# Kernel optimization log

Hardware: AMD Instinct MI355X
Metric: run time of the kernel (lower is better)

Reference implementation:

```python
import jax, jax.numpy as jnp
import numpy as np

N_NODES = 100000
D = 256
N_EDGES = 3200000
NEG_SLOPE = 0.01  # torch F.leaky_relu default


def setup_inputs() -> dict:
    key = jax.random.key(0)
    ks = jax.random.split(key, 5)
    x = jax.random.normal(ks[0], (N_NODES, D), dtype=jnp.float32)
    edge_rows = jax.random.randint(ks[1], (N_EDGES,), 0, N_NODES, dtype=jnp.int32)
    edge_cols = jax.random.randint(ks[2], (N_EDGES,), 0, N_NODES, dtype=jnp.int32)
    edge_vals = jax.random.uniform(ks[3], (N_EDGES,), dtype=jnp.float32)
    # Linear(dim, dim) with xavier_normal_ weight, default bias init ~ U(-1/sqrt(d), 1/sqrt(d))
    std = float(np.sqrt(2.0 / (D + D)))
    W_w = jax.random.normal(ks[4], (D, D), dtype=jnp.float32) * std
    W_b = jnp.zeros((D,), dtype=jnp.float32)
    return {"x": x, "edge_rows": edge_rows, "edge_cols": edge_cols,
            "edge_vals": edge_vals, "W_w": W_w, "W_b": W_b}


def reference(x, edge_rows, edge_cols, edge_vals, W_w, W_b):
    # h = W(x)  (torch Linear: x @ W^T + b)
    h = jnp.einsum('nd,ed->ne', x, W_w) + W_b  # [n, d]
    # SpMM: out[r] = sum_e A[r, c_e] * h[c_e]  via gather + segment_sum
    msgs = edge_vals[:, None] * h[edge_cols]  # [n_edges, d]
    agg = jax.ops.segment_sum(msgs, edge_rows, num_segments=x.shape[0])  # [n, d]
    return jnp.where(agg >= 0, agg, NEG_SLOPE * agg)
```

## Files before the change

### kernel.cpp

```cpp
#include <hip/hip_runtime.h>
#include <stdint.h>

#define DIM 256
#define NEG_SLOPE 0.01f

#define NBLK 512
#define MAXK 400
#define ROWS_PER_BUCKET 256

typedef float    vfloat4 __attribute__((ext_vector_type(4)));
typedef _Float16 vhalf4  __attribute__((ext_vector_type(4)));
typedef _Float16 half8   __attribute__((ext_vector_type(8)));
typedef float    floatx4 __attribute__((ext_vector_type(4)));
typedef unsigned int vuint2 __attribute__((ext_vector_type(2)));


#define MBM 128
#define MBN 64
#define MBK 32
#define MLDP 40

__global__ __launch_bounds__(256) void gemm_xwT_kernel(
        const float* __restrict__ x, const float* __restrict__ W,
        const float* __restrict__ bias, _Float16* __restrict__ h, int M) {
    __shared__ _Float16 Ax[MBM][MLDP];
    __shared__ _Float16 Bw[MBN][MLDP];

    const int tid  = (int)threadIdx.x;
    const int row0 = blockIdx.y * MBM;
    const int col0 = blockIdx.x * MBN;
    const int wid  = tid >> 6;
    const int lane = tid & 63;
    const int wr = wid >> 1;
    const int wc = wid & 1;
    const int fr = lane & 15;
    const int fk = (lane >> 4) * 8;

    const int arow = tid >> 1;
    const int ak   = (tid & 1) * 16;
    const int wrow = tid >> 2;
    const int wk   = (tid & 3) * 8;

    floatx4 acc[4][2];
#pragma unroll
    for (int m = 0; m < 4; ++m)
#pragma unroll
        for (int n = 0; n < 2; ++n) acc[m][n] = (floatx4){0.f, 0.f, 0.f, 0.f};

    for (int kk = 0; kk < DIM; kk += MBK) {
        {
            int grow = row0 + arow;
            const float* src = &x[(size_t)grow * DIM + kk + ak];
            half8 h0, h1;
            if (grow < M) {
                vfloat4 f0 = *(const vfloat4*)(src + 0);
                vfloat4 f1 = *(const vfloat4*)(src + 4);
                vfloat4 f2 = *(const vfloat4*)(src + 8);
                vfloat4 f3 = *(const vfloat4*)(src + 12);
                h0 = (half8){(_Float16)f0.x, (_Float16)f0.y, (_Float16)f0.z, (_Float16)f0.w,
                             (_Float16)f1.x, (_Float16)f1.y, (_Float16)f1.z, (_Float16)f1.w};
                h1 = (half8){(_Float16)f2.x, (_Float16)f2.y, (_Float16)f2.z, (_Float16)f2.w,
                             (_Float16)f3.x, (_Float16)f3.y, (_Float16)f3.z, (_Float16)f3.w};
            } else {
                h0 = (half8)(_Float16)0; h1 = (half8)(_Float16)0;
            }
            *(half8*)&Ax[arow][ak]     = h0;
            *(half8*)&Ax[arow][ak + 8] = h1;
        }
        {
            const float* src = &W[(size_t)(col0 + wrow) * DIM + kk + wk];
            vfloat4 f0 = *(const vfloat4*)(src + 0);
            vfloat4 f1 = *(const vfloat4*)(src + 4);
            half8 hb = (half8){(_Float16)f0.x, (_Float16)f0.y, (_Float16)f0.z, (_Float16)f0.w,
                               (_Float16)f1.x, (_Float16)f1.y, (_Float16)f1.z, (_Float16)f1.w};
            *(half8*)&Bw[wrow][wk] = hb;
        }
        __syncthreads();

        half8 a[4], b[2];
#pragma unroll
        for (int m = 0; m < 4; ++m)
            a[m] = *(const half8*)&Ax[wr * 64 + m * 16 + fr][fk];
#pragma unroll
        for (int n = 0; n < 2; ++n)
            b[n] = *(const half8*)&Bw[wc * 32 + n * 16 + fr][fk];
#pragma unroll
        for (int m = 0; m < 4; ++m)
#pragma unroll
            for (int n = 0; n < 2; ++n)
                acc[m][n] = __builtin_amdgcn_mfma_f32_16x16x32_f16(a[m], b[n], acc[m][n], 0, 0, 0);
        __syncthreads();
    }

#pragma unroll
    for (int m = 0; m < 4; ++m) {
#pragma unroll
        for (int n = 0; n < 2; ++n) {
            int col = col0 + wc * 32 + n * 16 + fr;
            float bv = bias[col];
#pragma unroll
            for (int j = 0; j < 4; ++j) {
                int row = row0 + wr * 64 + m * 16 + (lane >> 4) * 4 + j;
                if (row < M)
                    h[(size_t)row * DIM + col] = (_Float16)(acc[m][n][j] + bv);
            }
        }
    }
}


__device__ inline int wave_incl_scan(int v) {
    const int lane = threadIdx.x & 63;
#pragma unroll
    for (int off = 1; off < 64; off <<= 1) {
        int t = __shfl_up(v, off, 64);
        if (lane >= off) v += t;
    }
    return v;
}


__global__ __launch_bounds__(256) void hist2_kernel(const int* __restrict__ rows,
        int* __restrict__ hist2, int E, int K, int chunk) {
    __shared__ int lh[MAXK];
    const int tid = (int)threadIdx.x;
    const int b = (int)blockIdx.x;
    for (int i = tid; i < K; i += 256) lh[i] = 0;
    __syncthreads();
    const int beg = b * chunk;
    const int end = min(beg + chunk, E);
    for (int i = beg + tid; i < end; i += 256)
        atomicAdd(&lh[__builtin_nontemporal_load(&rows[i]) >> 8], 1);
    __syncthreads();
    for (int i = tid; i < K; i += 256) hist2[i * NBLK + b] = lh[i];
}

__global__ __launch_bounds__(256) void scanA_kernel(int* __restrict__ hist2,
        int* __restrict__ total, int K) {
    __shared__ int wtot[4];
    const int tid = (int)threadIdx.x;
    const int lane = tid & 63, wid = tid >> 6;
    const int k = (int)blockIdx.x;
    int* row = &hist2[k * NBLK];
    int v0 = row[tid * 2], v1 = row[tid * 2 + 1];
    int s = v0 + v1;
    int incl = wave_incl_scan(s);
    if (lane == 63) wtot[wid] = incl;
    __syncthreads();
    int woff = 0;
    for (int ww = 0; ww < wid; ++ww) woff += wtot[ww];
    int excl = woff + incl - s;
    row[tid * 2] = excl;
    row[tid * 2 + 1] = excl + v0;
    if (tid == 255) total[k] = woff + incl;
}

__global__ __launch_bounds__(64) void scanB_kernel(const int* __restrict__ total,
        int* __restrict__ bbase, int K) {
    const int lane = (int)threadIdx.x;
    int run = 0;
    for (int b = 0; b < K; b += 64) {
        int i = b + lane;
        int v = (i < K) ? total[i] : 0;
        int incl = wave_incl_scan(v);
        if (i < K) bbase[i] = run + incl - v;
        run += __shfl(incl, 63, 64);
    }
}

__global__ __launch_bounds__(256) void coarse_scatter_kernel(
        const int* __restrict__ rows, const int* __restrict__ cols,
        const float* __restrict__ vals, const int* __restrict__ hist2,
        const int* __restrict__ bbase, vuint2* __restrict__ coarse,
        int E, int K, int chunk) {
    __shared__ int cur[MAXK];
    const int tid = (int)threadIdx.x;
    const int b = (int)blockIdx.x;
    for (int i = tid; i < K; i += 256) cur[i] = bbase[i] + hist2[i * NBLK + b];
    __syncthreads();
    const int beg = b * chunk;
    const int end = min(beg + chunk, E);
    for (int i = beg + tid; i < end; i += 256) {
        int r = __builtin_nontemporal_load(&rows[i]);
        int c = __builtin_nontemporal_load(&cols[i]);
        float v = __builtin_nontemporal_load(&vals[i]);
        int pos = atomicAdd(&cur[r >> 8], 1);
        vuint2 rec;
        rec.x = ((unsigned)(r & 255) << 18) | (unsigned)c;
        rec.y = __float_as_uint(v);
        coarse[pos] = rec;
    }
}

__global__ __launch_bounds__(256) void fine_sort_kernel(
        const vuint2* __restrict__ coarse, const int* __restrict__ bbase,
        vuint2* __restrict__ sorted, int* __restrict__ offs,
        int N, int E, int K) {
    __shared__ int lh[ROWS_PER_BUCKET];
    __shared__ int wtot[4];
    const int tid = (int)threadIdx.x;
    const int lane = tid & 63, wid = tid >> 6;
    const int k = (int)blockIdx.x;
    const int row0 = k * ROWS_PER_BUCKET;
    const int beg = bbase[k];
    const int end = (k + 1 < K) ? bbase[k + 1] : E;
    lh[tid] = 0;
    __syncthreads();
    for (int j = beg + tid; j < end; j += 256)
        atomicAdd(&lh[coarse[j].x >> 18], 1);
    __syncthreads();
    int v = lh[tid];
    int incl = wave_incl_scan(v);
    if (lane == 63) wtot[wid] = incl;
    __syncthreads();
    int woff = 0;
    for (int ww = 0; ww < wid; ++ww) woff += wtot[ww];
    int excl = woff + incl - v;
    lh[tid] = beg + excl;
    if (row0 + tid < N) offs[row0 + tid] = beg + excl;
    __syncthreads();
    for (int j = beg + tid; j < end; j += 256) {
        vuint2 rec = __builtin_nontemporal_load(&coarse[j]);
        int pos = atomicAdd(&lh[rec.x >> 18], 1);
        sorted[pos] = rec;
    }
}


__global__ __launch_bounds__(256) void agg_kernel(
        const _Float16* __restrict__ h, const vuint2* __restrict__ sorted,
        const int* __restrict__ offs, float* __restrict__ out, int N, int E) {
    const int node = blockIdx.x * 4 + ((int)threadIdx.x >> 6);
    if (node >= N) return;
    const int lane = (int)threadIdx.x & 63;
    const int beg = offs[node];
    const int end = (node + 1 < N) ? offs[node + 1] : E;

    float4 acc0 = make_float4(0.f, 0.f, 0.f, 0.f);
    float4 acc1 = make_float4(0.f, 0.f, 0.f, 0.f);

    int j = beg;
    for (; j + 7 < end; j += 8) {
        vuint2 cv[8];
        vhalf4 hv[8];
#pragma unroll
        for (int u = 0; u < 8; ++u) cv[u] = __builtin_nontemporal_load(&sorted[j + u]);
#pragma unroll
        for (int u = 0; u < 8; ++u)
            hv[u] = *(const vhalf4*)(&h[(size_t)(cv[u].x & 0x3FFFF) * DIM + lane * 4]);
#pragma unroll
        for (int u = 0; u < 8; ++u) {
            float v = __uint_as_float(cv[u].y);
            float4* a = (u & 1) ? &acc1 : &acc0;
            a->x += v * (float)hv[u].x;
            a->y += v * (float)hv[u].y;
            a->z += v * (float)hv[u].z;
            a->w += v * (float)hv[u].w;
        }
    }
    for (; j < end; ++j) {
        vuint2 cv = __builtin_nontemporal_load(&sorted[j]);
        float v = __uint_as_float(cv.y);
        vhalf4 hv = *(const vhalf4*)(&h[(size_t)(cv.x & 0x3FFFF) * DIM + lane * 4]);
        acc0.x += v * (float)hv.x; acc0.y += v * (float)hv.y;
        acc0.z += v * (float)hv.z; acc0.w += v * (float)hv.w;
    }
    vfloat4 a;
    a.x = acc0.x + acc1.x;
    a.y = acc0.y + acc1.y;
    a.z = acc0.z + acc1.z;
    a.w = acc0.w + acc1.w;
    a.x = (a.x >= 0.f) ? a.x : NEG_SLOPE * a.x;
    a.y = (a.y >= 0.f) ? a.y : NEG_SLOPE * a.y;
    a.z = (a.z >= 0.f) ? a.z : NEG_SLOPE * a.z;
    a.w = (a.w >= 0.f) ? a.w : NEG_SLOPE * a.w;
    __builtin_nontemporal_store(a, (vfloat4*)(&out[(size_t)node * DIM + lane * 4]));
}


__global__ __launch_bounds__(256) void zero_f32_kernel(float* __restrict__ p, long long n) {
    long long i = (long long)blockIdx.x * blockDim.x + threadIdx.x;
    long long stride = (long long)gridDim.x * blockDim.x;
    for (; i < n; i += stride) p[i] = 0.0f;
}

__global__ __launch_bounds__(64) void edge_atomic_kernel(
        const int* __restrict__ rows, const int* __restrict__ cols,
        const float* __restrict__ vals, const _Float16* __restrict__ h,
        float* __restrict__ out, int E) {
    const int e = blockIdx.x;
    if (e >= E) return;
    const int lane = threadIdx.x;
    const int r = rows[e];
    const int c = cols[e];
    const float v = vals[e];
    vhalf4 hv = *(const vhalf4*)(&h[(size_t)c * DIM + lane * 4]);
    float* dst = &out[(size_t)r * DIM + lane * 4];
    atomicAdd(dst + 0, v * (float)hv.x);
    atomicAdd(dst + 1, v * (float)hv.y);
    atomicAdd(dst + 2, v * (float)hv.z);
    atomicAdd(dst + 3, v * (float)hv.w);
}

__global__ __launch_bounds__(256) void leaky_kernel(float* __restrict__ p, long long n) {
    long long i = (long long)blockIdx.x * blockDim.x + threadIdx.x;
    long long stride = (long long)gridDim.x * blockDim.x;
    for (; i < n; i += stride) {
        float v = p[i];
        p[i] = (v >= 0.f) ? v : NEG_SLOPE * v;
    }
}


extern "C" void kernel_launch(void* const* d_in, const int* in_sizes, int n_in,
                              void* d_out, int out_size, void* d_ws, size_t ws_size,
                              hipStream_t stream) {
    const float* x    = (const float*)d_in[0];
    const int*   erow = (const int*)d_in[1];
    const int*   ecol = (const int*)d_in[2];
    const float* eval_ = (const float*)d_in[3];
    const float* Ww   = (const float*)d_in[4];
    const float* Wb   = (const float*)d_in[5];
    float* out = (float*)d_out;

    const int N = in_sizes[0] / DIM;
    const int E = in_sizes[1];
    const int K = (N + ROWS_PER_BUCKET - 1) / ROWS_PER_BUCKET;
    const int chunk = (E + NBLK - 1) / NBLK;

    char* p = (char*)d_ws;
    _Float16* h = (_Float16*)p;                 p += (size_t)N * DIM * sizeof(_Float16);
    int* hist2 = (int*)p;                       p += (size_t)K * NBLK * sizeof(int);
    int* total = (int*)p;                       p += (size_t)((K + 63) & ~63) * sizeof(int);
    int* bbase = (int*)p;                       p += (size_t)((K + 63) & ~63) * sizeof(int);
    int* offs = (int*)p;                        p += (size_t)N * sizeof(int);
    uintptr_t up = ((uintptr_t)p + 15) & ~(uintptr_t)15;
    vuint2* sorted = (vuint2*)up;
    size_t need_full = (size_t)((char*)sorted - (char*)d_ws) + (size_t)E * sizeof(vuint2);
    size_t need_h = (size_t)N * DIM * sizeof(_Float16);
    bool coarse_fits = ((size_t)out_size * sizeof(float)) >= (size_t)E * sizeof(vuint2);

    dim3 ggrid(DIM / MBN, (N + MBM - 1) / MBM);

    if (ws_size >= need_full && K <= MAXK && coarse_fits && N <= (1 << 18)) {
        vuint2* coarse = (vuint2*)d_out;
        hist2_kernel<<<NBLK, 256, 0, stream>>>(erow, hist2, E, K, chunk);
        scanA_kernel<<<K, 256, 0, stream>>>(hist2, total, K);
        scanB_kernel<<<1, 64, 0, stream>>>(total, bbase, K);
        coarse_scatter_kernel<<<NBLK, 256, 0, stream>>>(erow, ecol, eval_, hist2,
                                                        bbase, coarse, E, K, chunk);
        fine_sort_kernel<<<K, 256, 0, stream>>>(coarse, bbase, sorted, offs, N, E, K);
        gemm_xwT_kernel<<<ggrid, 256, 0, stream>>>(x, Ww, Wb, h, N);
        agg_kernel<<<(N + 3) / 4, 256, 0, stream>>>(h, sorted, offs, out, N, E);
    } else if (ws_size >= need_h) {
        gemm_xwT_kernel<<<ggrid, 256, 0, stream>>>(x, Ww, Wb, h, N);
        zero_f32_kernel<<<2048, 256, 0, stream>>>(out, (long long)N * DIM);
        edge_atomic_kernel<<<E, 64, 0, stream>>>(erow, ecol, eval_, h, out, E);
        leaky_kernel<<<2048, 256, 0, stream>>>(out, (long long)N * DIM);
    }
}
```

Baseline: 420.1 us.

## Finer sort buckets, fuse bucket scan into consumers, stage fine sort in LDS

Halves the rows per bucket (256→128) and the number of scatter blocks (512→256), doubling the bucket count. The separate single-block scanB kernel is removed and each coarse_scatter and fine_sort block recomputes the bucket base prefix from the totals, saving one launch at the cost of redundant scans. Fine sort stages a bucket's records in a 48KB LDS buffer so coarse records are read from global memory once instead of twice. The aggregation loop is unrolled to 16 edges with 8/4 tails to keep more gathers in flight, raising register pressure.

```diff
diff --git a/kernel.cpp b/kernel.cpp
--- a/kernel.cpp
+++ b/kernel.cpp
@@ -4,9 +4,10 @@
 #define DIM 256
 #define NEG_SLOPE 0.01f
 
-#define NBLK 512
-#define MAXK 400
-#define ROWS_PER_BUCKET 256
+#define NBLK 256
+#define MAXK 800
+#define RPB 128
+#define FCAP 6144
 
 typedef float    vfloat4 __attribute__((ext_vector_type(4)));
 typedef _Float16 vhalf4  __attribute__((ext_vector_type(4)));
@@ -130,7 +131,7 @@
     const int beg = b * chunk;
     const int end = min(beg + chunk, E);
     for (int i = beg + tid; i < end; i += 256)
-        atomicAdd(&lh[__builtin_nontemporal_load(&rows[i]) >> 8], 1);
+        atomicAdd(&lh[__builtin_nontemporal_load(&rows[i]) >> 7], 1);
     __syncthreads();
     for (int i = tid; i < K; i += 256) hist2[i * NBLK + b] = lh[i];
 }
@@ -142,41 +143,38 @@
     const int lane = tid & 63, wid = tid >> 6;
     const int k = (int)blockIdx.x;
     int* row = &hist2[k * NBLK];
-    int v0 = row[tid * 2], v1 = row[tid * 2 + 1];
-    int s = v0 + v1;
-    int incl = wave_incl_scan(s);
+    int v = row[tid];
+    int incl = wave_incl_scan(v);
     if (lane == 63) wtot[wid] = incl;
     __syncthreads();
     int woff = 0;
     for (int ww = 0; ww < wid; ++ww) woff += wtot[ww];
-    int excl = woff + incl - s;
-    row[tid * 2] = excl;
-    row[tid * 2 + 1] = excl + v0;
+    row[tid] = woff + incl - v;
     if (tid == 255) total[k] = woff + incl;
-}
-
-__global__ __launch_bounds__(64) void scanB_kernel(const int* __restrict__ total,
-        int* __restrict__ bbase, int K) {
-    const int lane = (int)threadIdx.x;
-    int run = 0;
-    for (int b = 0; b < K; b += 64) {
-        int i = b + lane;
-        int v = (i < K) ? total[i] : 0;
-        int incl = wave_incl_scan(v);
-        if (i < K) bbase[i] = run + incl - v;
-        run += __shfl(incl, 63, 64);
-    }
 }
 
 __global__ __launch_bounds__(256) void coarse_scatter_kernel(
         const int* __restrict__ rows, const int* __restrict__ cols,
         const float* __restrict__ vals, const int* __restrict__ hist2,
-        const int* __restrict__ bbase, vuint2* __restrict__ coarse,
+        const int* __restrict__ total, vuint2* __restrict__ coarse,
         int E, int K, int chunk) {
+    __shared__ int bb[MAXK];
     __shared__ int cur[MAXK];
     const int tid = (int)threadIdx.x;
+    const int lane = tid & 63, wid = tid >> 6;
     const int b = (int)blockIdx.x;
-    for (int i = tid; i < K; i += 256) cur[i] = bbase[i] + hist2[i * NBLK + b];
+    if (wid == 0) {
+        int run = 0;
+        for (int base = 0; base < K; base += 64) {
+            int i = base + lane;
+            int v = (i < K) ? total[i] : 0;
+            int incl = wave_incl_scan(v);
+            if (i < K) bb[i] = run + incl - v;
+            run += __shfl(incl, 63, 64);
+        }
+    }
+    __syncthreads();
+    for (int i = tid; i < K; i += 256) cur[i] = bb[i] + hist2[i * NBLK + b];
     __syncthreads();
     const int beg = b * chunk;
     const int end = min(beg + chunk, E);
@@ -184,45 +182,83 @@
         int r = __builtin_nontemporal_load(&rows[i]);
         int c = __builtin_nontemporal_load(&cols[i]);
         float v = __builtin_nontemporal_load(&vals[i]);
-        int pos = atomicAdd(&cur[r >> 8], 1);
+        int pos = atomicAdd(&cur[r >> 7], 1);
         vuint2 rec;
-        rec.x = ((unsigned)(r & 255) << 18) | (unsigned)c;
+        rec.x = ((unsigned)(r & 127) << 18) | (unsigned)c;
         rec.y = __float_as_uint(v);
         coarse[pos] = rec;
     }
 }
 
 __global__ __launch_bounds__(256) void fine_sort_kernel(
-        const vuint2* __restrict__ coarse, const int* __restrict__ bbase,
+        const vuint2* __restrict__ coarse, const int* __restrict__ total,
         vuint2* __restrict__ sorted, int* __restrict__ offs,
         int N, int E, int K) {
-    __shared__ int lh[ROWS_PER_BUCKET];
-    __shared__ int wtot[4];
+    __shared__ vuint2 recs[FCAP];
+    __shared__ int bb[MAXK];
+    __shared__ int lh[RPB];
+    __shared__ int wtot0;
     const int tid = (int)threadIdx.x;
     const int lane = tid & 63, wid = tid >> 6;
     const int k = (int)blockIdx.x;
-    const int row0 = k * ROWS_PER_BUCKET;
-    const int beg = bbase[k];
-    const int end = (k + 1 < K) ? bbase[k + 1] : E;
-    lh[tid] = 0;
-    __syncthreads();
-    for (int j = beg + tid; j < end; j += 256)
-        atomicAdd(&lh[coarse[j].x >> 18], 1);
-    __syncthreads();
-    int v = lh[tid];
-    int incl = wave_incl_scan(v);
-    if (lane == 63) wtot[wid] = incl;
-    __syncthreads();
-    int woff = 0;
-    for (int ww = 0; ww < wid; ++ww) woff += wtot[ww];
-    int excl = woff + incl - v;
-    lh[tid] = beg + excl;
-    if (row0 + tid < N) offs[row0 + tid] = beg + excl;
-    __syncthreads();
-    for (int j = beg + tid; j < end; j += 256) {
-        vuint2 rec = __builtin_nontemporal_load(&coarse[j]);
-        int pos = atomicAdd(&lh[rec.x >> 18], 1);
-        sorted[pos] = rec;
+    const int row0 = k * RPB;
+
+    if (wid == 0) {
+        int run = 0;
+        for (int base = 0; base < K; base += 64) {
+            int i = base + lane;
+            int v = (i < K) ? total[i] : 0;
+            int incl = wave_incl_scan(v);
+            if (i < K) bb[i] = run + incl - v;
+            run += __shfl(incl, 63, 64);
+        }
+    }
+    if (tid < RPB) lh[tid] = 0;
+    __syncthreads();
+    const int beg = bb[k];
+    const int end = (k + 1 < K) ? bb[k + 1] : E;
+    const int cnt = end - beg;
+    const bool stage = (cnt <= FCAP);
+
+    if (stage) {
+        for (int j = beg + tid; j < end; j += 256) {
+            vuint2 rec = __builtin_nontemporal_load(&coarse[j]);
+            recs[j - beg] = rec;
+            atomicAdd(&lh[rec.x >> 18], 1);
+        }
+    } else {
+        for (int j = beg + tid; j < end; j += 256)
+            atomicAdd(&lh[coarse[j].x >> 18], 1);
+    }
+    __syncthreads();
+
+    int v = 0, incl = 0;
+    if (tid < RPB) {
+        v = lh[tid];
+        incl = wave_incl_scan(v);
+    }
+    if (tid == 63) wtot0 = incl;
+    __syncthreads();
+    if (tid >= 64 && tid < RPB) incl += wtot0;
+    if (tid < RPB) {
+        int e0 = beg + incl - v;
+        lh[tid] = e0;
+        if (row0 + tid < N) offs[row0 + tid] = e0;
+    }
+    __syncthreads();
+
+    if (stage) {
+        for (int idx = tid; idx < cnt; idx += 256) {
+            vuint2 rec = recs[idx];
+            int pos = atomicAdd(&lh[rec.x >> 18], 1);
+            sorted[pos] = rec;
+        }
+    } else {
+        for (int j = beg + tid; j < end; j += 256) {
+            vuint2 rec = __builtin_nontemporal_load(&coarse[j]);
+            int pos = atomicAdd(&lh[rec.x >> 18], 1);
+            sorted[pos] = rec;
+        }
     }
 }
 
@@ -240,7 +276,25 @@
     float4 acc1 = make_float4(0.f, 0.f, 0.f, 0.f);
 
     int j = beg;
-    for (; j + 7 < end; j += 8) {
+    for (; j + 15 < end; j += 16) {
+        vuint2 cv[16];
+        vhalf4 hv[16];
+#pragma unroll
+        for (int u = 0; u < 16; ++u) cv[u] = __builtin_nontemporal_load(&sorted[j + u]);
+#pragma unroll
+        for (int u = 0; u < 16; ++u)
+            hv[u] = *(const vhalf4*)(&h[(size_t)(cv[u].x & 0x3FFFF) * DIM + lane * 4]);
+#pragma unroll
+        for (int u = 0; u < 16; ++u) {
+            float v = __uint_as_float(cv[u].y);
+            float4* a = (u & 1) ? &acc1 : &acc0;
+            a->x += v * (float)hv[u].x;
+            a->y += v * (float)hv[u].y;
+            a->z += v * (float)hv[u].z;
+            a->w += v * (float)hv[u].w;
+        }
+    }
+    if (j + 7 < end) {
         vuint2 cv[8];
         vhalf4 hv[8];
 #pragma unroll
@@ -257,6 +311,26 @@
             a->z += v * (float)hv[u].z;
             a->w += v * (float)hv[u].w;
         }
+        j += 8;
+    }
+    if (j + 3 < end) {
+        vuint2 cv[4];
+        vhalf4 hv[4];
+#pragma unroll
+        for (int u = 0; u < 4; ++u) cv[u] = __builtin_nontemporal_load(&sorted[j + u]);
+#pragma unroll
+        for (int u = 0; u < 4; ++u)
+            hv[u] = *(const vhalf4*)(&h[(size_t)(cv[u].x & 0x3FFFF) * DIM + lane * 4]);
+#pragma unroll
+        for (int u = 0; u < 4; ++u) {
+            float v = __uint_as_float(cv[u].y);
+            float4* a = (u & 1) ? &acc1 : &acc0;
+            a->x += v * (float)hv[u].x;
+            a->y += v * (float)hv[u].y;
+            a->z += v * (float)hv[u].z;
+            a->w += v * (float)hv[u].w;
+        }
+        j += 4;
     }
     for (; j < end; ++j) {
         vuint2 cv = __builtin_nontemporal_load(&sorted[j]);
@@ -325,14 +399,13 @@
 
     const int N = in_sizes[0] / DIM;
     const int E = in_sizes[1];
-    const int K = (N + ROWS_PER_BUCKET - 1) / ROWS_PER_BUCKET;
+    const int K = (N + RPB - 1) / RPB;
     const int chunk = (E + NBLK - 1) / NBLK;
 
     char* p = (char*)d_ws;
     _Float16* h = (_Float16*)p;                 p += (size_t)N * DIM * sizeof(_Float16);
     int* hist2 = (int*)p;                       p += (size_t)K * NBLK * sizeof(int);
     int* total = (int*)p;                       p += (size_t)((K + 63) & ~63) * sizeof(int);
-    int* bbase = (int*)p;                       p += (size_t)((K + 63) & ~63) * sizeof(int);
     int* offs = (int*)p;                        p += (size_t)N * sizeof(int);
     uintptr_t up = ((uintptr_t)p + 15) & ~(uintptr_t)15;
     vuint2* sorted = (vuint2*)up;
@@ -346,10 +419,9 @@
         vuint2* coarse = (vuint2*)d_out;
         hist2_kernel<<<NBLK, 256, 0, stream>>>(erow, hist2, E, K, chunk);
         scanA_kernel<<<K, 256, 0, stream>>>(hist2, total, K);
-        scanB_kernel<<<1, 64, 0, stream>>>(total, bbase, K);
         coarse_scatter_kernel<<<NBLK, 256, 0, stream>>>(erow, ecol, eval_, hist2,
-                                                        bbase, coarse, E, K, chunk);
-        fine_sort_kernel<<<K, 256, 0, stream>>>(coarse, bbase, sorted, offs, N, E, K);
+                                                        total, coarse, E, K, chunk);
+        fine_sort_kernel<<<K, 256, 0, stream>>>(coarse, total, sorted, offs, N, E, K);
         gemm_xwT_kernel<<<ggrid, 256, 0, stream>>>(x, Ww, Wb, h, N);
         agg_kernel<<<(N + 3) / 4, 256, 0, stream>>>(h, sorted, offs, out, N, E);
     } else if (ws_size >= need_h) {
```

Result: slower. 432.4 us (+2.9%).
